# Kernel tuning notes

Hardware: AMD Instinct MI355X
Metric: run time of the kernel (lower is better)

The kernel has to match this reference:

```python
import jax, jax.numpy as jnp
import numpy as np

N_HEAD = 12

def setup_inputs() -> dict:
    key = jax.random.key(0)
    ks = jax.random.split(key, 5)
    B, T, C = 4, 2048, 768
    scale = 0.02
    return {
        "x": jax.random.normal(ks[0], (B, T, C), dtype=jnp.float32),
        "W_attn": jax.random.normal(ks[1], (C, 3 * C), dtype=jnp.float32) * scale,
        "b_attn": jax.random.normal(ks[2], (3 * C,), dtype=jnp.float32) * scale,
        "W_proj": jax.random.normal(ks[3], (C, C), dtype=jnp.float32) * scale,
        "b_proj": jax.random.normal(ks[4], (C,), dtype=jnp.float32) * scale,
    }

def reference(x, W_attn, b_attn, W_proj, b_proj):
    B, T, C = x.shape
    H = N_HEAD
    D = C // H  # head dim
    qkv = x @ W_attn + b_attn  # [B,T,3C]
    q, k, v = jnp.split(qkv, 3, axis=-1)
    # [B,H,T,D]
    q = q.reshape(B, T, H, D).transpose(0, 2, 1, 3)
    k = k.reshape(B, T, H, D).transpose(0, 2, 1, 3)
    v = v.reshape(B, T, H, D).transpose(0, 2, 1, 3)
    scores = jnp.einsum('bhqd,bhkd->bhqk', q, k) / jnp.sqrt(jnp.float32(D))
    causal = jnp.tril(jnp.ones((T, T), dtype=bool))
    scores = jnp.where(causal[None, None, :, :], scores, jnp.float32(-jnp.inf))
    attn = jax.nn.softmax(scores, axis=-1)
    out = jnp.einsum('bhqk,bhkd->bhqd', attn, v)  # [B,H,T,D]
    out = out.transpose(0, 2, 1, 3).reshape(B, T, C)
    return out @ W_proj + b_proj
```

## Files before the change

kernel.cpp:

```cpp
#include <hip/hip_runtime.h>

typedef float f32x4 __attribute__((ext_vector_type(4)));
typedef __bf16 bf16x8 __attribute__((ext_vector_type(8)));
typedef unsigned short u16x8 __attribute__((ext_vector_type(8)));
typedef unsigned short u16x4 __attribute__((ext_vector_type(4)));

#define MFMA16(a, b, c) __builtin_amdgcn_mfma_f32_16x16x32_bf16((a), (b), (c), 0, 0, 0)

__device__ __forceinline__ unsigned short f2bf(float f) {
    __bf16 h = (__bf16)f;
    union { __bf16 h; unsigned short u; } c; c.h = h;
    return c.u;
}

__device__ __forceinline__ void gload_lds16(const unsigned short* g, unsigned short* l) {
    __builtin_amdgcn_global_load_lds(
        (const __attribute__((address_space(1))) unsigned int*)g,
        (__attribute__((address_space(3))) unsigned int*)l, 16, 0, 0);
}

__global__ void k_convert_bf16(const float* __restrict__ in,
                               unsigned short* __restrict__ out, int n) {
    int i = (blockIdx.x * 256 + threadIdx.x) * 4;
    if (i + 3 < n) {
        float4 v = *reinterpret_cast<const float4*>(in + i);
        ushort4 o;
        o.x = f2bf(v.x); o.y = f2bf(v.y); o.z = f2bf(v.z); o.w = f2bf(v.w);
        *reinterpret_cast<ushort4*>(out + i) = o;
    }
}

__global__ void k_transpose_bf16(const float* __restrict__ in,
                                 unsigned short* __restrict__ out, int R, int C) {
    __shared__ unsigned short tile[32][33];
    int bx = blockIdx.x * 32;
    int by = blockIdx.y * 32;
    int tx = threadIdx.x;
    int ty = threadIdx.y;
    #pragma unroll
    for (int i = ty; i < 32; i += 8)
        tile[i][tx] = f2bf(in[(size_t)(by + i) * C + bx + tx]);
    __syncthreads();
    #pragma unroll
    for (int i = ty; i < 32; i += 8)
        out[(size_t)(bx + i) * R + by + tx] = tile[tx][i];
}

template<int EPI>
__global__ __launch_bounds__(EPI == 0 ? 512 : 256) void k_gemm_bt(
    const unsigned short* __restrict__ A,
    const unsigned short* __restrict__ Bt,
    const float* __restrict__ bias,
    unsigned short* __restrict__ Qo,
    unsigned short* __restrict__ Ko,
    unsigned short* __restrict__ Vto,
    float* __restrict__ Co,
    int K)
{
    constexpr int THREADS = (EPI == 0) ? 512 : 256;
    constexpr int BM      = (EPI == 0) ? 256 : 128;
    constexpr int ROWSTEP = THREADS / 8;
    __shared__ unsigned short SM[(BM + 128) * 64];
    unsigned short* As = SM;
    unsigned short* Bs = SM + BM * 64;
    const int nwg = gridDim.x * gridDim.y;
    const int bid0 = blockIdx.y * gridDim.x + blockIdx.x;
    const int logical = (bid0 & 7) * (nwg >> 3) + (bid0 >> 3);
    const int bm = logical / gridDim.x;
    const int bn = logical % gridDim.x;
    const int tid = threadIdx.x;
    const int w = tid >> 6, l = tid & 63;
    const int wm = w >> 1, wn = w & 1;
    const int ln = l & 15, kb = l >> 4;

    f32x4 acc[4][4];
    #pragma unroll
    for (int i = 0; i < 4; ++i)
        #pragma unroll
        for (int j = 0; j < 4; ++j)
            #pragma unroll
            for (int r = 0; r < 4; ++r) acc[i][j][r] = 0.f;

    const unsigned short* Ab = A + (size_t)(bm * BM) * K;
    const unsigned short* Bb = Bt + (size_t)(bn * 128) * K;

    const int srow = tid >> 3;
    const int sslot = tid & 7;
    const int csw = (sslot ^ (srow & 7)) * 8;

    for (int k0 = 0; k0 < K; k0 += 64) {
        #pragma unroll
        for (int j = 0; j < BM / ROWSTEP; ++j) {
            const int r = j * ROWSTEP + srow;
            gload_lds16(&Ab[(size_t)r * K + k0 + csw], &As[r * 64 + sslot * 8]);
        }
        #pragma unroll
        for (int j = 0; j < 128 / ROWSTEP; ++j) {
            const int r = j * ROWSTEP + srow;
            gload_lds16(&Bb[(size_t)r * K + k0 + csw], &Bs[r * 64 + sslot * 8]);
        }
        __syncthreads();
        #pragma unroll
        for (int kh = 0; kh < 2; ++kh) {
            bf16x8 af[4], bfr[4];
            #pragma unroll
            for (int mt = 0; mt < 4; ++mt) {
                const int row = wm * 64 + mt * 16 + ln;
                const int slot = ((kh << 2) | kb) ^ (row & 7);
                af[mt] = *reinterpret_cast<const bf16x8*>(&As[row * 64 + slot * 8]);
            }
            #pragma unroll
            for (int nt = 0; nt < 4; ++nt) {
                const int row = wn * 64 + nt * 16 + ln;
                const int slot = ((kh << 2) | kb) ^ (row & 7);
                bfr[nt] = *reinterpret_cast<const bf16x8*>(&Bs[row * 64 + slot * 8]);
            }
            #pragma unroll
            for (int mt = 0; mt < 4; ++mt)
                #pragma unroll
                for (int nt = 0; nt < 4; ++nt)
                    acc[mt][nt] = MFMA16(af[mt], bfr[nt], acc[mt][nt]);
        }
        __syncthreads();
    }

    const float SC = 0.1803368801111204f;

    if (EPI == 0 && bn >= 12) {
        unsigned short* Ts = SM;
        const int cl_w = wn * 64;
        #pragma unroll
        for (int hh2 = 0; hh2 < 2; ++hh2) {
            if ((wm >> 1) == hh2) {
                #pragma unroll
                for (int mt = 0; mt < 4; ++mt) {
                    #pragma unroll
                    for (int nt = 0; nt < 4; ++nt) {
                        const int cl = cl_w + nt * 16 + ln;
                        const float bv = bias[bn * 128 + cl];
                        #pragma unroll
                        for (int r = 0; r < 4; ++r) {
                            const int rl = (wm & 1) * 64 + mt * 16 + kb * 4 + r;
                            const int pos = cl * 128 + ((((rl >> 3) ^ (cl & 7)) << 3) | (rl & 7));
                            Ts[pos] = f2bf(acc[mt][nt][r] + bv);
                        }
                    }
                }
            }
            __syncthreads();
            {
                const int cl = tid >> 2;
                const int col = bn * 128 + cl;
                const int cc = col - 1536;
                const int hh = cc >> 6, dd = cc & 63;
                #pragma unroll
                for (int j8 = 0; j8 < 4; ++j8) {
                    const int rb = (tid & 3) * 4 + j8;
                    u16x8 val = *reinterpret_cast<const u16x8*>(&Ts[cl * 128 + ((rb ^ (cl & 7)) << 3)]);
                    const int tg = bm * BM + hh2 * 128 + rb * 8;
                    const int bb = tg >> 11;
                    const int tloc = tg & 2047;
                    const int grp = tloc & ~31;
                    const int jj = (tloc >> 3) & 3;
                    const int tlo = grp + 8 * ((2 * jj) & 3) + 4 * (jj >> 1);
                    const int thi = grp + 8 * ((2 * jj + 1) & 3) + 4 * (jj >> 1);
                    unsigned short* basep = &Vto[((size_t)((bb * 12 + hh) * 64 + dd)) * 2048];
                    *reinterpret_cast<u16x4*>(basep + tlo) =
                        __builtin_shufflevector(val, val, 0, 1, 2, 3);
                    *reinterpret_cast<u16x4*>(basep + thi) =
                        __builtin_shufflevector(val, val, 4, 5, 6, 7);
                }
            }
            __syncthreads();
        }
        return;
    }

    #pragma unroll
    for (int mt = 0; mt < 4; ++mt) {
        #pragma unroll
        for (int nt = 0; nt < 4; ++nt) {
            const int col = bn * 128 + wn * 64 + nt * 16 + ln;
            #pragma unroll
            for (int r = 0; r < 4; ++r) {
                const int row = bm * BM + wm * 64 + mt * 16 + kb * 4 + r;
                float v = acc[mt][nt][r] + bias[col];
                if (EPI == 0) {
                    int cc = col >= 768 ? col - 768 : col;
                    int h = cc >> 6, d = cc & 63;
                    int b = row >> 11, t = row & 2047;
                    if (col < 768)
                        Qo[((size_t)((b * 12 + h) * 2048 + t)) * 64 + d] = f2bf(v * SC);
                    else
                        Ko[((size_t)((b * 12 + h) * 2048 + t)) * 64 + d] = f2bf(v);
                } else {
                    Co[(size_t)row * 768 + col] = v;
                }
            }
        }
    }
}

__global__ __launch_bounds__(256) void k_attn(
    const unsigned short* __restrict__ Q,
    const unsigned short* __restrict__ Kk,
    const unsigned short* __restrict__ Vt,
    unsigned short* __restrict__ Oo)
{
    __shared__ unsigned short SMEM[4 * 4096];
    const int bid0 = blockIdx.x;
    const int xcd = bid0 & 7;
    const int loc = bid0 >> 3;
    const int qb = 15 - (loc / 6);
    const int bh = xcd * 6 + (loc % 6);
    const int tid = threadIdx.x;
    const int w = tid >> 6, l = tid & 63;
    const int ln = l & 15, kb = l >> 4;
    const int kbq = kb * 4;
    const int b = bh / 12, h = bh - b * 12;
    const int q0w = qb * 128 + w * 32;

    const unsigned short* Qb = Q + (size_t)bh * 2048 * 64;
    const unsigned short* Kb = Kk + (size_t)bh * 2048 * 64;
    const unsigned short* Vb = Vt + (size_t)bh * 64 * 2048;

    bf16x8 qf[2][2];
    #pragma unroll
    for (int qn = 0; qn < 2; ++qn) {
        const unsigned short* qr = &Qb[(size_t)(q0w + qn * 16 + ln) * 64 + kb * 8];
        qf[qn][0] = *reinterpret_cast<const bf16x8*>(qr);
        qf[qn][1] = *reinterpret_cast<const bf16x8*>(qr + 32);
    }

    bf16x8 vones;
    #pragma unroll
    for (int e = 0; e < 8; ++e) vones[e] = (__bf16)1.0f;
    const f32x4 fzero = {0.f, 0.f, 0.f, 0.f};

    f32x4 oaccT[2][4];
    f32x4 den[2];
    #pragma unroll
    for (int qn = 0; qn < 2; ++qn) {
        #pragma unroll
        for (int r = 0; r < 4; ++r) den[qn][r] = 0.f;
        #pragma unroll
        for (int dt = 0; dt < 4; ++dt)
            #pragma unroll
            for (int r = 0; r < 4; ++r) oaccT[qn][dt][r] = 0.f;
    }

    const int lb = ln & 7;
    const int aR0 = ln * 64 + (kb ^ lb) * 8;
    const int aR1 = ln * 64 + ((4 | kb) ^ lb) * 8;

    const int srow = tid >> 3;
    const int sslot = tid & 7;
    const int csw = (sslot ^ (srow & 7)) * 8;
    const int lastkt = (q0w + 31) >> 6;

    #define STAGE(kt_, buf_)                                                        \
        {                                                                           \
            const int kb_ = (kt_) * 64;                                             \
            _Pragma("unroll")                                                       \
            for (int j = 0; j < 2; ++j) {                                           \
                const int r = j * 32 + srow;                                        \
                gload_lds16(&Kb[(size_t)(kb_ + r) * 64 + csw],                      \
                            &SMEM[(buf_) * 4096 + r * 64 + sslot * 8]);             \
                gload_lds16(&Vb[(size_t)r * 2048 + kb_ + csw],                      \
                            &SMEM[8192 + (buf_) * 4096 + r * 64 + sslot * 8]);      \
            }                                                                       \
        }

    #define COMPUTE(kt_, BUF)                                                       \
        if ((kt_) <= lastkt) {                                                      \
            bf16x8 kf[4][2];                                                        \
            _Pragma("unroll")                                                       \
            for (int km = 0; km < 4; ++km) {                                        \
                kf[km][0] = *reinterpret_cast<const bf16x8*>(                       \
                    &SMEM[(BUF) * 4096 + km * 1024 + aR0]);                         \
                kf[km][1] = *reinterpret_cast<const bf16x8*>(                       \
                    &SMEM[(BUF) * 4096 + km * 1024 + aR1]);                         \
            }                                                                       \
            f32x4 st[4][2];                                                         \
            _Pragma("unroll")                                                       \
            for (int km = 0; km < 4; ++km)                                          \
                _Pragma("unroll")                                                   \
                for (int qn = 0; qn < 2; ++qn) {                                    \
                    st[km][qn] = MFMA16(kf[km][0], qf[qn][0], fzero);               \
                    st[km][qn] = MFMA16(kf[km][1], qf[qn][1], st[km][qn]);          \
                }                                                                   \
            bf16x8 vf[4][2];                                                        \
            _Pragma("unroll")                                                       \
            for (int dt = 0; dt < 4; ++dt) {                                        \
                vf[dt][0] = *reinterpret_cast<const bf16x8*>(                       \
                    &SMEM[8192 + (BUF) * 4096 + dt * 1024 + aR0]);                  \
                vf[dt][1] = *reinterpret_cast<const bf16x8*>(                       \
                    &SMEM[8192 + (BUF) * 4096 + dt * 1024 + aR1]);                  \
            }                                                                       \
            if ((kt_) == lastkt) {                                                  \
                const int kbase_ = (kt_) * 64;                                      \
                _Pragma("unroll")                                                   \
                for (int qn = 0; qn < 2; ++qn) {                                    \
                    const int qrow = q0w + qn * 16 + ln;                            \
                    _Pragma("unroll")                                               \
                    for (int km = 0; km < 4; ++km)                                  \
                        _Pragma("unroll")                                           \
                        for (int r = 0; r < 4; ++r) {                               \
                            float sv = st[km][qn][r];                               \
                            const int key = kbase_ + km * 16 + kbq + r;             \
                            sv = (key <= qrow) ? sv : -1e30f;                       \
                            st[km][qn][r] = __builtin_amdgcn_exp2f(sv);             \
                        }                                                           \
                }                                                                   \
            } else {                                                                \
                _Pragma("unroll")                                                   \
                for (int qn = 0; qn < 2; ++qn)                                      \
                    _Pragma("unroll")                                               \
                    for (int km = 0; km < 4; ++km)                                  \
                        _Pragma("unroll")                                           \
                        for (int r = 0; r < 4; ++r)                                 \
                            st[km][qn][r] =                                         \
                                __builtin_amdgcn_exp2f(st[km][qn][r]);              \
            }                                                                       \
            bf16x8 pa[2][2];                                                        \
            _Pragma("unroll")                                                       \
            for (int qn = 0; qn < 2; ++qn)                                          \
                _Pragma("unroll")                                                   \
                for (int kh = 0; kh < 2; ++kh) {                                    \
                    bf16x8 t;                                                       \
                    _Pragma("unroll")                                               \
                    for (int r = 0; r < 4; ++r) {                                   \
                        t[r]     = (__bf16)st[2 * kh][qn][r];                       \
                        t[r + 4] = (__bf16)st[2 * kh + 1][qn][r];                   \
                    }                                                               \
                    pa[qn][kh] = t;                                                 \
                }                                                                   \
            _Pragma("unroll")                                                       \
            for (int qn = 0; qn < 2; ++qn) {                                        \
                _Pragma("unroll")                                                   \
                for (int dt = 0; dt < 4; ++dt) {                                    \
                    oaccT[qn][dt] = MFMA16(pa[qn][0], vf[dt][0], oaccT[qn][dt]);    \
                    oaccT[qn][dt] = MFMA16(pa[qn][1], vf[dt][1], oaccT[qn][dt]);    \
                }                                                                   \
                den[qn] = MFMA16(pa[qn][0], vones, den[qn]);                        \
                den[qn] = MFMA16(pa[qn][1], vones, den[qn]);                        \
            }                                                                       \
        }

    STAGE(0, 0);

    for (int s = 0; s <= qb; ++s) {
        const int ktA = 2 * s;
        const int ktB = 2 * s + 1;
        __syncthreads();
        STAGE(ktB, 1);
        COMPUTE(ktA, 0);
        __syncthreads();
        if (s < qb) STAGE(ktA + 2, 0);
        COMPUTE(ktB, 1);
    }

    #pragma unroll
    for (int qn = 0; qn < 2; ++qn) {
        #pragma unroll
        for (int r = 0; r < 4; ++r) {
            const float inv = 1.0f / den[qn][r];
            const int t = q0w + qn * 16 + kbq + r;
            #pragma unroll
            for (int dt = 0; dt < 4; ++dt)
                Oo[((size_t)(b * 2048 + t)) * 768 + h * 64 + dt * 16 + ln] =
                    f2bf(oaccT[qn][dt][r] * inv);
        }
    }
    #undef STAGE
    #undef COMPUTE
}

extern "C" void kernel_launch(void* const* d_in, const int* in_sizes, int n_in,
                              void* d_out, int out_size, void* d_ws, size_t ws_size,
                              hipStream_t stream) {
    const float* x      = (const float*)d_in[0];
    const float* W_attn = (const float*)d_in[1];
    const float* b_attn = (const float*)d_in[2];
    const float* W_proj = (const float*)d_in[3];
    const float* b_proj = (const float*)d_in[4];
    float* out = (float*)d_out;

    char* ws = (char*)d_ws;
    const size_t SZ_X  = (size_t)8192 * 768 * 2;
    const size_t SZ_WA = (size_t)2304 * 768 * 2;
    const size_t SZ_WP = (size_t)768 * 768 * 2;
    const size_t SZ_T  = (size_t)8192 * 768 * 2;

    unsigned short* x_bf = (unsigned short*)(ws);
    unsigned short* wa_t = (unsigned short*)(ws + SZ_X);
    unsigned short* wp_t = (unsigned short*)(ws + SZ_X + SZ_WA);
    unsigned short* Qb   = (unsigned short*)(ws + SZ_X + SZ_WA + SZ_WP);
    unsigned short* Kb   = (unsigned short*)(ws + SZ_X + SZ_WA + SZ_WP + SZ_T);
    unsigned short* Vtb  = (unsigned short*)(ws + SZ_X + SZ_WA + SZ_WP + 2 * SZ_T);
    unsigned short* attn_o = x_bf;

    k_convert_bf16<<<6144, 256, 0, stream>>>(x, x_bf, 8192 * 768);
    dim3 tb(32, 8);
    k_transpose_bf16<<<dim3(2304 / 32, 768 / 32), tb, 0, stream>>>(W_attn, wa_t, 768, 2304);
    k_transpose_bf16<<<dim3(768 / 32, 768 / 32), tb, 0, stream>>>(W_proj, wp_t, 768, 768);
    k_gemm_bt<0><<<dim3(18, 32), 512, 0, stream>>>(x_bf, wa_t, b_attn, Qb, Kb, Vtb, nullptr, 768);
    k_attn<<<768, 256, 0, stream>>>(Qb, Kb, Vtb, attn_o);
    k_gemm_bt<1><<<dim3(6, 64), 256, 0, stream>>>(attn_o, wp_t, b_proj, nullptr, nullptr, nullptr, out, 768);
}
```

Measured before the change: 118.3 us.

## Double-buffer GEMM K-tiles with BK=32 and interleave attention query-block order

The GEMM main loop now prefetches the next 32-wide K slice into a second LDS buffer while computing on the current one. This uses one barrier per iteration and a new XOR swizzle for the narrower rows, aiming to overlap global loads with MFMA work. The attention kernel's block-to-query-block mapping now alternates long and short causal rows instead of running heaviest first, to change load balancing. Halving the K tile doubles loop iterations and barrier count, and the new schedule order could hurt tail balance.

Measured after the change: 131.3 us. 11.0% more time.

```diff
diff --git a/kernel.cpp b/kernel.cpp
--- a/kernel.cpp
+++ b/kernel.cpp
@@ -59,10 +59,8 @@
 {
     constexpr int THREADS = (EPI == 0) ? 512 : 256;
     constexpr int BM      = (EPI == 0) ? 256 : 128;
-    constexpr int ROWSTEP = THREADS / 8;
-    __shared__ unsigned short SM[(BM + 128) * 64];
-    unsigned short* As = SM;
-    unsigned short* Bs = SM + BM * 64;
+    constexpr int RS      = THREADS / 4;
+    __shared__ unsigned short SM[2 * BM * 32 + 2 * 128 * 32];
     const int nwg = gridDim.x * gridDim.y;
     const int bid0 = blockIdx.y * gridDim.x + blockIdx.x;
     const int logical = (bid0 & 7) * (nwg >> 3) + (bid0 >> 3);
@@ -84,45 +82,51 @@
     const unsigned short* Ab = A + (size_t)(bm * BM) * K;
     const unsigned short* Bb = Bt + (size_t)(bn * 128) * K;
 
-    const int srow = tid >> 3;
-    const int sslot = tid & 7;
-    const int csw = (sslot ^ (srow & 7)) * 8;
-
-    for (int k0 = 0; k0 < K; k0 += 64) {
-        #pragma unroll
-        for (int j = 0; j < BM / ROWSTEP; ++j) {
-            const int r = j * ROWSTEP + srow;
-            gload_lds16(&Ab[(size_t)r * K + k0 + csw], &As[r * 64 + sslot * 8]);
-        }
-        #pragma unroll
-        for (int j = 0; j < 128 / ROWSTEP; ++j) {
-            const int r = j * ROWSTEP + srow;
-            gload_lds16(&Bb[(size_t)r * K + k0 + csw], &Bs[r * 64 + sslot * 8]);
-        }
+    const int srow = tid >> 2;
+    const int sslot = tid & 3;
+    const int scs = (sslot ^ ((srow >> 1) & 3)) * 8;
+
+    const int slot8 = (kb ^ ((ln >> 1) & 3)) * 8;
+    const int aBase = (wm * 64 + ln) * 32 + slot8;
+    const int bBase = 2 * BM * 32 + (wn * 64 + ln) * 32 + slot8;
+
+    #define GSTAGE(t_, buf_)                                                        \
+        {                                                                           \
+            const int k0_ = (t_) * 32;                                              \
+            _Pragma("unroll")                                                       \
+            for (int j = 0; j < BM / RS; ++j) {                                     \
+                const int r = j * RS + srow;                                        \
+                gload_lds16(&Ab[(size_t)r * K + k0_ + scs],                         \
+                            &SM[(buf_) * BM * 32 + r * 32 + sslot * 8]);            \
+            }                                                                       \
+            _Pragma("unroll")                                                       \
+            for (int j = 0; j < 128 / RS; ++j) {                                    \
+                const int r = j * RS + srow;                                        \
+                gload_lds16(&Bb[(size_t)r * K + k0_ + scs],                         \
+                            &SM[2 * BM * 32 + (buf_) * 128 * 32 + r * 32 + sslot * 8]); \
+            }                                                                       \
+        }
+
+    const int NT = K >> 5;
+    GSTAGE(0, 0);
+    for (int t = 0; t < NT; ++t) {
         __syncthreads();
-        #pragma unroll
-        for (int kh = 0; kh < 2; ++kh) {
-            bf16x8 af[4], bfr[4];
+        if (t + 1 < NT) GSTAGE(t + 1, (t + 1) & 1);
+        const int buf = t & 1;
+        bf16x8 af[4], bfr[4];
+        #pragma unroll
+        for (int mt = 0; mt < 4; ++mt)
+            af[mt] = *reinterpret_cast<const bf16x8*>(&SM[buf * BM * 32 + mt * 512 + aBase]);
+        #pragma unroll
+        for (int nt = 0; nt < 4; ++nt)
+            bfr[nt] = *reinterpret_cast<const bf16x8*>(&SM[buf * 128 * 32 + nt * 512 + bBase]);
+        #pragma unroll
+        for (int mt = 0; mt < 4; ++mt)
             #pragma unroll
-            for (int mt = 0; mt < 4; ++mt) {
-                const int row = wm * 64 + mt * 16 + ln;
-                const int slot = ((kh << 2) | kb) ^ (row & 7);
-                af[mt] = *reinterpret_cast<const bf16x8*>(&As[row * 64 + slot * 8]);
-            }
-            #pragma unroll
-            for (int nt = 0; nt < 4; ++nt) {
-                const int row = wn * 64 + nt * 16 + ln;
-                const int slot = ((kh << 2) | kb) ^ (row & 7);
-                bfr[nt] = *reinterpret_cast<const bf16x8*>(&Bs[row * 64 + slot * 8]);
-            }
-            #pragma unroll
-            for (int mt = 0; mt < 4; ++mt)
-                #pragma unroll
-                for (int nt = 0; nt < 4; ++nt)
-                    acc[mt][nt] = MFMA16(af[mt], bfr[nt], acc[mt][nt]);
-        }
-        __syncthreads();
-    }
+            for (int nt = 0; nt < 4; ++nt)
+                acc[mt][nt] = MFMA16(af[mt], bfr[nt], acc[mt][nt]);
+    }
+    __syncthreads();
 
     const float SC = 0.1803368801111204f;
 
@@ -199,6 +203,7 @@
             }
         }
     }
+    #undef GSTAGE
 }
 
 __global__ __launch_bounds__(256) void k_attn(
@@ -211,7 +216,8 @@
     const int bid0 = blockIdx.x;
     const int xcd = bid0 & 7;
     const int loc = bid0 >> 3;
-    const int qb = 15 - (loc / 6);
+    const int jq = loc / 6;
+    const int qb = (jq & 1) ? (jq >> 1) : (15 - (jq >> 1));
     const int bh = xcd * 6 + (loc % 6);
     const int tid = threadIdx.x;
     const int w = tid >> 6, l = tid & 63;
```
